# Kernel optimization log

Measured on AMD Instinct MI355X. Metric: run time of the kernel, lower is better.

Reference implementation:

```python
import jax, jax.numpy as jnp
import numpy as np

H = 1024  # lstm hidden size

def setup_inputs() -> dict:
    key = jax.random.key(0)
    ks = jax.random.split(key, 8)
    B, T, V, E = 64, 512, 32000, 512
    s = 0.05
    return {
        "x": jax.random.randint(ks[0], (B, T), 0, V),
        "emb": jax.random.normal(ks[1], (V, E), jnp.float32) * s,
        "W_ih": jax.random.normal(ks[2], (4 * H, E), jnp.float32) * s,
        "W_hh": jax.random.normal(ks[3], (4 * H, H), jnp.float32) * s,
        "b_ih": jax.random.normal(ks[4], (4 * H,), jnp.float32) * s,
        "b_hh": jax.random.normal(ks[5], (4 * H,), jnp.float32) * s,
        "W_fc": jax.random.normal(ks[6], (1, H), jnp.float32) * s,
        "b_fc": jax.random.normal(ks[7], (1,), jnp.float32) * s,
    }

def _lstm_final_h(xe, W_ih, W_hh, b_ih, b_hh):
    # xe: [B,T,E]. Precompute input projections for all steps (same math as per-step).
    B = xe.shape[0]
    xproj = jnp.einsum('bte,ge->btg', xe, W_ih) + b_ih + b_hh  # [B,T,4H]
    xproj = jnp.swapaxes(xproj, 0, 1)                          # [T,B,4H]

    def step(carry, xp_t):
        h, c = carry
        gates = xp_t + h @ W_hh.T                              # [B,4H]
        i, f, g, o = jnp.split(gates, 4, axis=-1)              # torch gate order i,f,g,o
        i = jax.nn.sigmoid(i); f = jax.nn.sigmoid(f)
        g = jnp.tanh(g);       o = jax.nn.sigmoid(o)
        c = f * c + i * g
        h = o * jnp.tanh(c)
        return (h, c), None

    h0 = jnp.zeros((B, H), xe.dtype)
    c0 = jnp.zeros((B, H), xe.dtype)
    (h, c), _ = jax.lax.scan(step, (h0, c0), xproj)
    return h                                                   # [B,H] final hidden

def reference(x, emb, W_ih, W_hh, b_ih, b_hh, W_fc, b_fc):
    xe = emb[x]                                                # [B,T,E]
    h = _lstm_final_h(xe, W_ih, W_hh, b_ih, b_hh)              # [B,H]
    out = h @ W_fc.T + b_fc                                    # [B,1]
    # torch: fc applied to h of shape [1,B,H] -> [1,B,1]; dropout in eval is identity
    return jax.nn.sigmoid(out)[None, :, :]                     # [1,B,1]
```

## Files before the change

kernel.cpp:

```cpp
#include <hip/hip_runtime.h>
#include <hip/hip_bf16.h>
#include <cstdint>

typedef __bf16 bf16_t;
typedef __bf16 bf16x8 __attribute__((ext_vector_type(8)));
typedef float  f32x4  __attribute__((ext_vector_type(4)));
typedef unsigned long long u64;
typedef unsigned int u32;
typedef unsigned short u16;

#define T_SEQ 512
#define HROT  64
#define NCOLG 64
#define NCLQ  4

#define MFMA(a, b, c) __builtin_amdgcn_mfma_f32_16x16x32_bf16((a), (b), (c), 0, 0, 0)

static __device__ __forceinline__ u64 ldA8(const u64* p) {
  return __hip_atomic_load(p, __ATOMIC_RELAXED, __HIP_MEMORY_SCOPE_AGENT);
}
static __device__ __forceinline__ bf16x8 ld16(const bf16_t* p) {
  return *(const bf16x8*)p;
}

__global__ void gather_xe(const int* __restrict__ x, const float* __restrict__ emb,
                          bf16_t* __restrict__ xe) {
  const int row = blockIdx.x;
  const int b = row & 63, t = row >> 6;
  const int tok = x[b * 512 + t];
  const float4* src = (const float4*)(emb + (size_t)tok * 512);
  float4 a = src[threadIdx.x * 2], c = src[threadIdx.x * 2 + 1];
  bf16x8 v;
  v[0] = (bf16_t)a.x; v[1] = (bf16_t)a.y; v[2] = (bf16_t)a.z; v[3] = (bf16_t)a.w;
  v[4] = (bf16_t)c.x; v[5] = (bf16_t)c.y; v[6] = (bf16_t)c.z; v[7] = (bf16_t)c.w;
  *(bf16x8*)(xe + (size_t)row * 512 + threadIdx.x * 8) = v;
}

__global__ void cvt_f32_bf16(const float* __restrict__ s, bf16_t* __restrict__ d, int n8) {
  int i = blockIdx.x * blockDim.x + threadIdx.x;
  if (i >= n8) return;
  const float4* sp = (const float4*)s;
  float4 a = sp[2 * (size_t)i], b = sp[2 * (size_t)i + 1];
  bf16x8 v;
  v[0] = (bf16_t)a.x; v[1] = (bf16_t)a.y; v[2] = (bf16_t)a.z; v[3] = (bf16_t)a.w;
  v[4] = (bf16_t)b.x; v[5] = (bf16_t)b.y; v[6] = (bf16_t)b.z; v[7] = (bf16_t)b.w;
  *(bf16x8*)(d + 8 * (size_t)i) = v;
}

__global__ __launch_bounds__(512, 1) void lstm_seq(
    const bf16_t* __restrict__ xe,
    const bf16_t* __restrict__ wihb,
    const float* __restrict__ whh,
    const float* __restrict__ bih, const float* __restrict__ bhh,
    const float* __restrict__ wfc, const float* __restrict__ bfc,
    bf16_t* __restrict__ hb,
    u32* __restrict__ flags,
    float* __restrict__ out) {
  __shared__ bf16_t whh_s[64][1032];
  __shared__ f32x4 red_s[7][4][64];
  const int tid = threadIdx.x, bid = blockIdx.x;
  const int lane = tid & 63, w = tid >> 6;
  const int clq = (bid & 7) >> 1;
  const int colg = ((bid >> 3) << 1) | (bid & 1);
  u32* flg = flags + clq * 64;

  {
    const int r = tid >> 3, sub = tid & 7;
    const int grow = (r >> 4) * 1024 + colg * 16 + (r & 15);
    const float4* s = (const float4*)(whh + (size_t)grow * 1024 + sub * 128);
    bf16_t* d = &whh_s[r][sub * 128];
#pragma unroll 8
    for (int u = 0; u < 32; ++u) {
      float4 f = s[u];
      d[u * 4 + 0] = (bf16_t)f.x; d[u * 4 + 1] = (bf16_t)f.y;
      d[u * 4 + 2] = (bf16_t)f.z; d[u * 4 + 3] = (bf16_t)f.w;
    }
  }
  __syncthreads();

  const int rloc = lane & 15, kg = lane >> 4;
  const int col = colg * 16 + rloc;
  const int brow = clq * 16 + rloc;

  const float bI = bih[col] + bhh[col];
  const float bF = bih[1024 + col] + bhh[1024 + col];
  const float bG = bih[2048 + col] + bhh[2048 + col];
  const float bO = bih[3072 + col] + bhh[3072 + col];

  const bf16_t* wB0 = wihb + ((size_t)(0 * 1024 + col)) * 512 + w * 64 + kg * 8;
  const bf16_t* wB1 = wihb + ((size_t)(1 * 1024 + col)) * 512 + w * 64 + kg * 8;
  const bf16_t* wB2 = wihb + ((size_t)(2 * 1024 + col)) * 512 + w * 64 + kg * 8;
  const bf16_t* wB3 = wihb + ((size_t)(3 * 1024 + col)) * 512 + w * 64 + kg * 8;
  const bf16_t* hB0 = &whh_s[ 0 + rloc][w * 128 + kg * 8];
  const bf16_t* hB1 = &whh_s[16 + rloc][w * 128 + kg * 8];
  const bf16_t* hB2 = &whh_s[32 + rloc][w * 128 + kg * 8];
  const bf16_t* hB3 = &whh_s[48 + rloc][w * 128 + kg * 8];

  float cs[4] = {0.f, 0.f, 0.f, 0.f};

  for (int t = 0; t < T_SEQ; ++t) {
    f32x4 A0 = {0.f, 0.f, 0.f, 0.f}, A1 = A0, A2 = A0, A3 = A0;

    const bf16_t* ax = xe + ((size_t)t * 64 + brow) * 512 + w * 64 + kg * 8;
#define XE_PART                                            \
    _Pragma("unroll")                                      \
    for (int kk = 0; kk < 2; ++kk) {                       \
      bf16x8 a = ld16(ax + kk * 32);                       \
      A0 = MFMA(a, ld16(wB0 + kk * 32), A0);               \
      A1 = MFMA(a, ld16(wB1 + kk * 32), A1);               \
      A2 = MFMA(a, ld16(wB2 + kk * 32), A2);               \
      A3 = MFMA(a, ld16(wB3 + kk * 32), A3);               \
    }
    if (w != 1) { XE_PART }

    if (t) {
      if (w == 1) {
        const u32 tgt = (u32)t;
        u32 v = __hip_atomic_load(flg + lane, __ATOMIC_RELAXED, __HIP_MEMORY_SCOPE_AGENT);
        while (!__all(v >= tgt)) {
          __builtin_amdgcn_s_sleep(1);
          v = __hip_atomic_load(flg + lane, __ATOMIC_RELAXED, __HIP_MEMORY_SCOPE_AGENT);
        }
      }
      __syncthreads();
      asm volatile("" ::: "memory");
    }
    if (w == 1) { XE_PART }
#undef XE_PART

    const bf16_t* ah = hb + (size_t)(t & (HROT - 1)) * 65536 +
                       (size_t)brow * 1024 + w * 128 + kg * 8;
#pragma unroll
    for (int kk = 0; kk < 4; ++kk) {
      bf16x8 a = __builtin_nontemporal_load((const bf16x8*)(ah + kk * 32));
      A0 = MFMA(a, ld16(hB0 + kk * 32), A0);
      A1 = MFMA(a, ld16(hB1 + kk * 32), A1);
      A2 = MFMA(a, ld16(hB2 + kk * 32), A2);
      A3 = MFMA(a, ld16(hB3 + kk * 32), A3);
    }

    if (w) {
      red_s[w - 1][0][lane] = A0; red_s[w - 1][1][lane] = A1;
      red_s[w - 1][2][lane] = A2; red_s[w - 1][3][lane] = A3;
    }
    __syncthreads();
    if (w == 0) {
#pragma unroll
      for (int q = 0; q < 7; ++q) {
        A0 += red_s[q][0][lane]; A1 += red_s[q][1][lane];
        A2 += red_s[q][2][lane]; A3 += red_s[q][3][lane];
      }
    }
    __syncthreads();

    if (w == 0) {
      u16* hn = (u16*)(hb + (size_t)((t + 1) & (HROT - 1)) * 65536) +
                (size_t)(clq * 16 + kg * 4) * 1024 + col;
#pragma unroll
      for (int r = 0; r < 4; ++r) {
        const float gi = A0[r] + bI, gf = A1[r] + bF, gg = A2[r] + bG, go = A3[r] + bO;
        const float ii = 1.f / (1.f + __expf(-gi));
        const float ff = 1.f / (1.f + __expf(-gf));
        const float gv = tanhf(gg);
        const float oo = 1.f / (1.f + __expf(-go));
        cs[r] = ff * cs[r] + ii * gv;
        const float hv = oo * tanhf(cs[r]);
        const bf16_t hvb = (bf16_t)hv;
        __hip_atomic_store(hn + (size_t)r * 1024, __builtin_bit_cast(u16, hvb),
                           __ATOMIC_RELAXED, __HIP_MEMORY_SCOPE_AGENT);
      }
      asm volatile("s_waitcnt vmcnt(0)" ::: "memory");
      if (lane == 0)
        __hip_atomic_store(flg + colg, (u32)(t + 1), __ATOMIC_RELAXED,
                           __HIP_MEMORY_SCOPE_AGENT);
    }
  }

  if (colg != 0) return;
  if (w == 0) {
    u32 v = __hip_atomic_load(flg + lane, __ATOMIC_RELAXED, __HIP_MEMORY_SCOPE_AGENT);
    while (!__all(v >= (u32)T_SEQ)) {
      __builtin_amdgcn_s_sleep(1);
      v = __hip_atomic_load(flg + lane, __ATOMIC_RELAXED, __HIP_MEMORY_SCOPE_AGENT);
    }
  }
  __syncthreads();
  if (tid < 64) {
    const int bth = tid >> 2, part = tid & 3;
    const int gb = clq * 16 + bth;
    const u64* hp = (const u64*)(hb + (size_t)gb * 1024 + part * 256);
    const float* wp = wfc + part * 256;
    float s = 0.f;
    for (int i = 0; i < 64; ++i) {
      union { u64 u; bf16_t h[4]; } xv;
      xv.u = ldA8(hp + i);
      s += (float)xv.h[0] * wp[i * 4] + (float)xv.h[1] * wp[i * 4 + 1] +
           (float)xv.h[2] * wp[i * 4 + 2] + (float)xv.h[3] * wp[i * 4 + 3];
    }
    s += __shfl_xor(s, 1);
    s += __shfl_xor(s, 2);
    if (part == 0) out[gb] = 1.f / (1.f + __expf(-(s + bfc[0])));
  }
}

extern "C" void kernel_launch(void* const* d_in, const int* in_sizes, int n_in,
                              void* d_out, int out_size, void* d_ws, size_t ws_size,
                              hipStream_t stream) {
  const int* x = (const int*)d_in[0];
  const float* emb = (const float*)d_in[1];
  const float* wih = (const float*)d_in[2];
  const float* whh = (const float*)d_in[3];
  const float* bih = (const float*)d_in[4];
  const float* bhh = (const float*)d_in[5];
  const float* wfc = (const float*)d_in[6];
  const float* bfc = (const float*)d_in[7];
  float* out = (float*)d_out;

  char* ws = (char*)d_ws;
  bf16_t* xe = (bf16_t*)ws;
  bf16_t* wihb = (bf16_t*)(ws + 33554432);
  bf16_t* hb = (bf16_t*)(ws + 33554432 + 4194304);
  u32* flags = (u32*)(ws + 33554432 + 4194304 + 8388608);

  hipMemsetAsync(hb, 0, 131072, stream);
  hipMemsetAsync(flags, 0, 1024, stream);
  gather_xe<<<32768, 64, 0, stream>>>(x, emb, xe);
  cvt_f32_bf16<<<1024, 256, 0, stream>>>(wih, wihb, 262144);

  void* args[] = {(void*)&xe, (void*)&wihb, (void*)&whh, (void*)&bih, (void*)&bhh,
                  (void*)&wfc, (void*)&bfc, (void*)&hb, (void*)&flags, (void*)&out};
  hipLaunchCooperativeKernel((const void*)lstm_seq, dim3(256), dim3(512), args, 0, stream);
}
```

Measured before the change: 3.380 ms.

## Replace flag-based step sync with tagged h words and double buffering

Each hidden value is now stored as a 32-bit word that packs the bf16 value with a step tag. Consumers poll the data itself until every tag matches, which removes the separate flag write, the vmcnt wait, the flag spin and one block barrier per step. The h ring shrinks from 64 slots to 2. The gate activations also switch to fast rcp-based sigmoid and tanh. The cost is doubled h traffic, since 32 bits are sent per value, and a double buffer that relies on tags to prevent overwrite races.

```diff
diff --git a/kernel.cpp b/kernel.cpp
--- a/kernel.cpp
+++ b/kernel.cpp
@@ -10,9 +10,7 @@
 typedef unsigned short u16;
 
 #define T_SEQ 512
-#define HROT  64
-#define NCOLG 64
-#define NCLQ  4
+#define TAGMASK 0x0000FFFF0000FFFFull
 
 #define MFMA(a, b, c) __builtin_amdgcn_mfma_f32_16x16x32_bf16((a), (b), (c), 0, 0, 0)
 
@@ -21,6 +19,12 @@
 }
 static __device__ __forceinline__ bf16x8 ld16(const bf16_t* p) {
   return *(const bf16x8*)p;
+}
+static __device__ __forceinline__ float sigm(float x) {
+  return __builtin_amdgcn_rcpf(1.f + __expf(-x));
+}
+static __device__ __forceinline__ float tanh_f(float x) {
+  return 2.f * __builtin_amdgcn_rcpf(1.f + __expf(-2.f * x)) - 1.f;
 }
 
 __global__ void gather_xe(const int* __restrict__ x, const float* __restrict__ emb,
@@ -53,8 +57,7 @@
     const float* __restrict__ whh,
     const float* __restrict__ bih, const float* __restrict__ bhh,
     const float* __restrict__ wfc, const float* __restrict__ bfc,
-    bf16_t* __restrict__ hb,
-    u32* __restrict__ flags,
+    u32* __restrict__ hw,
     float* __restrict__ out) {
   __shared__ bf16_t whh_s[64][1032];
   __shared__ f32x4 red_s[7][4][64];
@@ -62,7 +65,6 @@
   const int lane = tid & 63, w = tid >> 6;
   const int clq = (bid & 7) >> 1;
   const int colg = ((bid >> 3) << 1) | (bid & 1);
-  u32* flg = flags + clq * 64;
 
   {
     const int r = tid >> 3, sub = tid & 7;
@@ -102,42 +104,51 @@
     f32x4 A0 = {0.f, 0.f, 0.f, 0.f}, A1 = A0, A2 = A0, A3 = A0;
 
     const bf16_t* ax = xe + ((size_t)t * 64 + brow) * 512 + w * 64 + kg * 8;
-#define XE_PART                                            \
-    _Pragma("unroll")                                      \
-    for (int kk = 0; kk < 2; ++kk) {                       \
-      bf16x8 a = ld16(ax + kk * 32);                       \
-      A0 = MFMA(a, ld16(wB0 + kk * 32), A0);               \
-      A1 = MFMA(a, ld16(wB1 + kk * 32), A1);               \
-      A2 = MFMA(a, ld16(wB2 + kk * 32), A2);               \
-      A3 = MFMA(a, ld16(wB3 + kk * 32), A3);               \
-    }
-    if (w != 1) { XE_PART }
-
-    if (t) {
-      if (w == 1) {
-        const u32 tgt = (u32)t;
-        u32 v = __hip_atomic_load(flg + lane, __ATOMIC_RELAXED, __HIP_MEMORY_SCOPE_AGENT);
-        while (!__all(v >= tgt)) {
-          __builtin_amdgcn_s_sleep(1);
-          v = __hip_atomic_load(flg + lane, __ATOMIC_RELAXED, __HIP_MEMORY_SCOPE_AGENT);
-        }
-      }
-      __syncthreads();
-      asm volatile("" ::: "memory");
-    }
-    if (w == 1) { XE_PART }
-#undef XE_PART
-
-    const bf16_t* ah = hb + (size_t)(t & (HROT - 1)) * 65536 +
-                       (size_t)brow * 1024 + w * 128 + kg * 8;
-#pragma unroll
-    for (int kk = 0; kk < 4; ++kk) {
-      bf16x8 a = __builtin_nontemporal_load((const bf16x8*)(ah + kk * 32));
-      A0 = MFMA(a, ld16(hB0 + kk * 32), A0);
-      A1 = MFMA(a, ld16(hB1 + kk * 32), A1);
-      A2 = MFMA(a, ld16(hB2 + kk * 32), A2);
-      A3 = MFMA(a, ld16(hB3 + kk * 32), A3);
-    }
+#pragma unroll
+    for (int kk = 0; kk < 2; ++kk) {
+      bf16x8 a = ld16(ax + kk * 32);
+      A0 = MFMA(a, ld16(wB0 + kk * 32), A0);
+      A1 = MFMA(a, ld16(wB1 + kk * 32), A1);
+      A2 = MFMA(a, ld16(wB2 + kk * 32), A2);
+      A3 = MFMA(a, ld16(wB3 + kk * 32), A3);
+    }
+
+    const u64* hp = (const u64*)hw + (size_t)(t & 1) * 32768 +
+                    (size_t)brow * 512 + w * 64 + kg * 4;
+    u64 d0, d1, d2, d3, d4, d5, d6, d7, d8, d9, da, db, dc, dd, de, df;
+    {
+      const u64 tagpat = (u64)(u32)t * 0x0000000100000001ull;
+      for (;;) {
+        d0 = ldA8(hp +  0); d1 = ldA8(hp +  1); d2 = ldA8(hp +  2); d3 = ldA8(hp +  3);
+        d4 = ldA8(hp + 16); d5 = ldA8(hp + 17); d6 = ldA8(hp + 18); d7 = ldA8(hp + 19);
+        d8 = ldA8(hp + 32); d9 = ldA8(hp + 33); da = ldA8(hp + 34); db = ldA8(hp + 35);
+        dc = ldA8(hp + 48); dd = ldA8(hp + 49); de = ldA8(hp + 50); df = ldA8(hp + 51);
+        u64 diff = ((d0 ^ tagpat) | (d1 ^ tagpat) | (d2 ^ tagpat) | (d3 ^ tagpat) |
+                    (d4 ^ tagpat) | (d5 ^ tagpat) | (d6 ^ tagpat) | (d7 ^ tagpat) |
+                    (d8 ^ tagpat) | (d9 ^ tagpat) | (da ^ tagpat) | (db ^ tagpat) |
+                    (dc ^ tagpat) | (dd ^ tagpat) | (de ^ tagpat) | (df ^ tagpat)) & TAGMASK;
+        if (__all(diff == 0)) break;
+        __builtin_amdgcn_s_sleep(2);
+      }
+    }
+
+#define HKK(kk, e0, e1, e2, e3)                                                  \
+    {                                                                            \
+      union { u32 u[4]; bf16x8 v; } a;                                           \
+      a.u[0] = (u32)((e0 >> 16) & 0xFFFFu) | (u32)((e0 >> 48) << 16);            \
+      a.u[1] = (u32)((e1 >> 16) & 0xFFFFu) | (u32)((e1 >> 48) << 16);            \
+      a.u[2] = (u32)((e2 >> 16) & 0xFFFFu) | (u32)((e2 >> 48) << 16);            \
+      a.u[3] = (u32)((e3 >> 16) & 0xFFFFu) | (u32)((e3 >> 48) << 16);            \
+      A0 = MFMA(a.v, ld16(hB0 + kk * 32), A0);                                   \
+      A1 = MFMA(a.v, ld16(hB1 + kk * 32), A1);                                   \
+      A2 = MFMA(a.v, ld16(hB2 + kk * 32), A2);                                   \
+      A3 = MFMA(a.v, ld16(hB3 + kk * 32), A3);                                   \
+    }
+    HKK(0, d0, d1, d2, d3)
+    HKK(1, d4, d5, d6, d7)
+    HKK(2, d8, d9, da, db)
+    HKK(3, dc, dd, de, df)
+#undef HKK
 
     if (w) {
       red_s[w - 1][0][lane] = A0; red_s[w - 1][1][lane] = A1;
@@ -150,56 +161,53 @@
         A0 += red_s[q][0][lane]; A1 += red_s[q][1][lane];
         A2 += red_s[q][2][lane]; A3 += red_s[q][3][lane];
       }
-    }
-    __syncthreads();
-
-    if (w == 0) {
-      u16* hn = (u16*)(hb + (size_t)((t + 1) & (HROT - 1)) * 65536) +
+      u32* hn = hw + (size_t)((t + 1) & 1) * 65536 +
                 (size_t)(clq * 16 + kg * 4) * 1024 + col;
+      const u32 tag = (u32)(t + 1);
 #pragma unroll
       for (int r = 0; r < 4; ++r) {
         const float gi = A0[r] + bI, gf = A1[r] + bF, gg = A2[r] + bG, go = A3[r] + bO;
-        const float ii = 1.f / (1.f + __expf(-gi));
-        const float ff = 1.f / (1.f + __expf(-gf));
-        const float gv = tanhf(gg);
-        const float oo = 1.f / (1.f + __expf(-go));
-        cs[r] = ff * cs[r] + ii * gv;
-        const float hv = oo * tanhf(cs[r]);
+        const float ii = sigm(gi), ff = sigm(gf), oo = sigm(go);
+        cs[r] = ff * cs[r] + ii * tanh_f(gg);
+        const float hv = oo * tanh_f(cs[r]);
         const bf16_t hvb = (bf16_t)hv;
-        __hip_atomic_store(hn + (size_t)r * 1024, __builtin_bit_cast(u16, hvb),
+        const u32 word = ((u32)__builtin_bit_cast(u16, hvb) << 16) | tag;
+        __hip_atomic_store(hn + (size_t)r * 1024, word,
                            __ATOMIC_RELAXED, __HIP_MEMORY_SCOPE_AGENT);
       }
-      asm volatile("s_waitcnt vmcnt(0)" ::: "memory");
-      if (lane == 0)
-        __hip_atomic_store(flg + colg, (u32)(t + 1), __ATOMIC_RELAXED,
-                           __HIP_MEMORY_SCOPE_AGENT);
     }
   }
 
   if (colg != 0) return;
-  if (w == 0) {
-    u32 v = __hip_atomic_load(flg + lane, __ATOMIC_RELAXED, __HIP_MEMORY_SCOPE_AGENT);
-    while (!__all(v >= (u32)T_SEQ)) {
-      __builtin_amdgcn_s_sleep(1);
-      v = __hip_atomic_load(flg + lane, __ATOMIC_RELAXED, __HIP_MEMORY_SCOPE_AGENT);
-    }
-  }
-  __syncthreads();
   if (tid < 64) {
     const int bth = tid >> 2, part = tid & 3;
     const int gb = clq * 16 + bth;
-    const u64* hp = (const u64*)(hb + (size_t)gb * 1024 + part * 256);
+    const u64* hp = (const u64*)hw + (size_t)gb * 512 + part * 128;
     const float* wp = wfc + part * 256;
+    const u64 tagpat = (u64)(u32)T_SEQ * 0x0000000100000001ull;
     float s = 0.f;
-    for (int i = 0; i < 64; ++i) {
-      union { u64 u; bf16_t h[4]; } xv;
-      xv.u = ldA8(hp + i);
-      s += (float)xv.h[0] * wp[i * 4] + (float)xv.h[1] * wp[i * 4 + 1] +
-           (float)xv.h[2] * wp[i * 4 + 2] + (float)xv.h[3] * wp[i * 4 + 3];
+    for (int blk = 0; blk < 16; ++blk) {
+      u64 d[8];
+      for (;;) {
+        u64 diff = 0;
+#pragma unroll
+        for (int i = 0; i < 8; ++i) {
+          d[i] = ldA8(hp + blk * 8 + i);
+          diff |= (d[i] ^ tagpat) & TAGMASK;
+        }
+        if (diff == 0) break;
+        __builtin_amdgcn_s_sleep(2);
+      }
+#pragma unroll
+      for (int i = 0; i < 8; ++i) {
+        const float h0 = (float)__builtin_bit_cast(bf16_t, (u16)((d[i] >> 16) & 0xFFFFu));
+        const float h1 = (float)__builtin_bit_cast(bf16_t, (u16)(d[i] >> 48));
+        s += h0 * wp[blk * 16 + 2 * i] + h1 * wp[blk * 16 + 2 * i + 1];
+      }
     }
     s += __shfl_xor(s, 1);
     s += __shfl_xor(s, 2);
-    if (part == 0) out[gb] = 1.f / (1.f + __expf(-(s + bfc[0])));
+    if (part == 0) out[gb] = sigm(s + bfc[0]);
   }
 }
 
@@ -219,15 +227,13 @@
   char* ws = (char*)d_ws;
   bf16_t* xe = (bf16_t*)ws;
   bf16_t* wihb = (bf16_t*)(ws + 33554432);
-  bf16_t* hb = (bf16_t*)(ws + 33554432 + 4194304);
-  u32* flags = (u32*)(ws + 33554432 + 4194304 + 8388608);
-
-  hipMemsetAsync(hb, 0, 131072, stream);
-  hipMemsetAsync(flags, 0, 1024, stream);
+  u32* hw = (u32*)(ws + 33554432 + 4194304);
+
+  hipMemsetAsync(hw, 0, 262144, stream);
   gather_xe<<<32768, 64, 0, stream>>>(x, emb, xe);
   cvt_f32_bf16<<<1024, 256, 0, stream>>>(wih, wihb, 262144);
 
   void* args[] = {(void*)&xe, (void*)&wihb, (void*)&whh, (void*)&bih, (void*)&bhh,
-                  (void*)&wfc, (void*)&bfc, (void*)&hb, (void*)&flags, (void*)&out};
+                  (void*)&wfc, (void*)&bfc, (void*)&hw, (void*)&out};
   hipLaunchCooperativeKernel((const void*)lstm_seq, dim3(256), dim3(512), args, 0, stream);
 }
```

New measurement: 9.182 ms. 172% more time.
